# Optimization experiments

Hardware: AMD Instinct MI355X
Metric: run time of the kernel (lower is better)

Reference implementation:

```python
import jax, jax.numpy as jnp
import numpy as np

DIM = 16777216


def spu(z):
    # SPU(x) = x^2 - 0.5 for x >= 0, sigmoid(-x) - 1 for x < 0
    return jnp.where(z >= 0, z * z - 0.5, jax.nn.sigmoid(-z) - 1.0)


def setup_inputs() -> dict:
    key = jax.random.key(0)
    kx, kl, ku = jax.random.split(key, 3)
    x = jax.random.normal(kx, (1, DIM), dtype=jnp.float32)
    l_in = jax.random.normal(kl, (1, DIM), dtype=jnp.float32)
    # guarantee l <= u, with sign crossings so all three branches are exercised
    u_in = l_in + 2.0 * jax.random.uniform(ku, (1, DIM), dtype=jnp.float32)
    return {"x": x, "l_in": l_in, "u_in": u_in}


def reference(x, l_in, u_in):
    x_out = spu(x)
    spu_l = spu(l_in)
    spu_u = spu(u_in)
    # 3-way piecewise box bounds (vectorized _1D_box_bounds):
    #   l >= 0: (spu(l), spu(u)); u <= 0: (spu(u), spu(l)); else: (-0.5, spu(u))
    l_out = jnp.where(l_in >= 0, spu_l, jnp.where(u_in <= 0, spu_u, -0.5))
    u_out = jnp.where(u_in <= 0, spu_l, spu_u)
    return (x_out, l_out, u_out)
```

## Files before the change

### kernel.cpp

```cpp
#include <hip/hip_runtime.h>


typedef float v4f __attribute__((ext_vector_type(4)));

__device__ __forceinline__ float spu_fast(float z) {
    float e   = __expf(z);
    float neg = __builtin_amdgcn_rcpf(1.0f + e) - 1.0f;
    float pos = fmaf(z, z, -0.5f);
    return (z >= 0.0f) ? pos : neg;
}

__global__ __launch_bounds__(256)
void spu_box_kernel(const float* __restrict__ x,
                    const float* __restrict__ l_in,
                    const float* __restrict__ u_in,
                    float* __restrict__ x_out,
                    float* __restrict__ l_out,
                    float* __restrict__ u_out,
                    int n4)
{
    int i = blockIdx.x * blockDim.x + threadIdx.x;
    if (i >= n4) return;

    v4f xv = ((const v4f*)x)[i];
    v4f lv = ((const v4f*)l_in)[i];
    v4f uv = ((const v4f*)u_in)[i];

    v4f xo, lo, uo;

    #pragma unroll
    for (int k = 0; k < 4; ++k) {
        float xs = xv[k];
        float ls = lv[k];
        float us = uv[k];

        float sx = spu_fast(xs);
        float sl = spu_fast(ls);
        float su = spu_fast(us);

        lo[k] = (ls >= 0.0f) ? sl : ((us <= 0.0f) ? su : -0.5f);
        uo[k] = (us <= 0.0f) ? sl : su;
        xo[k] = sx;
    }

    __builtin_nontemporal_store(xo, (v4f*)x_out + i);
    __builtin_nontemporal_store(lo, (v4f*)l_out + i);
    __builtin_nontemporal_store(uo, (v4f*)u_out + i);
}

__global__ void spu_box_tail(const float* __restrict__ x,
                             const float* __restrict__ l_in,
                             const float* __restrict__ u_in,
                             float* __restrict__ x_out,
                             float* __restrict__ l_out,
                             float* __restrict__ u_out,
                             int start, int n)
{
    int i = start + blockIdx.x * blockDim.x + threadIdx.x;
    if (i >= n) return;
    float xs = x[i], ls = l_in[i], us = u_in[i];
    float sx = spu_fast(xs), sl = spu_fast(ls), su = spu_fast(us);
    x_out[i] = sx;
    l_out[i] = (ls >= 0.0f) ? sl : ((us <= 0.0f) ? su : -0.5f);
    u_out[i] = (us <= 0.0f) ? sl : su;
}

extern "C" void kernel_launch(void* const* d_in, const int* in_sizes, int n_in,
                              void* d_out, int out_size, void* d_ws, size_t ws_size,
                              hipStream_t stream) {
    const float* x    = (const float*)d_in[0];
    const float* l_in = (const float*)d_in[1];
    const float* u_in = (const float*)d_in[2];

    const int n = in_sizes[0];
    float* out   = (float*)d_out;
    float* x_out = out;
    float* l_out = out + n;
    float* u_out = out + 2 * (size_t)n;

    const int n4 = n / 4;
    const int block = 256;
    const int grid = (n4 + block - 1) / block;
    spu_box_kernel<<<grid, block, 0, stream>>>(x, l_in, u_in, x_out, l_out, u_out, n4);

    const int tail_start = n4 * 4;
    if (tail_start < n) {
        const int tail = n - tail_start;
        spu_box_tail<<<(tail + 63) / 64, 64, 0, stream>>>(x, l_in, u_in,
                                                          x_out, l_out, u_out,
                                                          tail_start, n);
    }
}
```

Measured before the change: 343.2 us.

## Use grid-stride loop with two-way unroll and drop nontemporal stores

Replaces the one-thread-per-vec4 launch with a grid capped at 2048 blocks that walks the data in a grid-stride loop, processing two vec4 elements per iteration so more loads are in flight per thread. It also swaps the nontemporal stores for ordinary stores. The goal is lower block scheduling overhead and more memory-level parallelism in this bandwidth-bound kernel. The cost is fewer resident waves overall and possible cache pollution from the regular stores.

```diff
diff --git a/kernel.cpp b/kernel.cpp
--- a/kernel.cpp
+++ b/kernel.cpp
@@ -10,42 +10,50 @@
     return (z >= 0.0f) ? pos : neg;
 }
 
-__global__ __launch_bounds__(256)
-void spu_box_kernel(const float* __restrict__ x,
-                    const float* __restrict__ l_in,
-                    const float* __restrict__ u_in,
-                    float* __restrict__ x_out,
-                    float* __restrict__ l_out,
-                    float* __restrict__ u_out,
-                    int n4)
-{
-    int i = blockIdx.x * blockDim.x + threadIdx.x;
-    if (i >= n4) return;
-
-    v4f xv = ((const v4f*)x)[i];
-    v4f lv = ((const v4f*)l_in)[i];
-    v4f uv = ((const v4f*)u_in)[i];
-
-    v4f xo, lo, uo;
-
+__device__ __forceinline__ void spu_box_v4(v4f xv, v4f lv, v4f uv,
+                                           v4f& xo, v4f& lo, v4f& uo) {
     #pragma unroll
     for (int k = 0; k < 4; ++k) {
-        float xs = xv[k];
-        float ls = lv[k];
-        float us = uv[k];
-
+        float xs = xv[k], ls = lv[k], us = uv[k];
         float sx = spu_fast(xs);
         float sl = spu_fast(ls);
         float su = spu_fast(us);
-
         lo[k] = (ls >= 0.0f) ? sl : ((us <= 0.0f) ? su : -0.5f);
         uo[k] = (us <= 0.0f) ? sl : su;
         xo[k] = sx;
     }
+}
 
-    __builtin_nontemporal_store(xo, (v4f*)x_out + i);
-    __builtin_nontemporal_store(lo, (v4f*)l_out + i);
-    __builtin_nontemporal_store(uo, (v4f*)u_out + i);
+__global__ __launch_bounds__(256)
+void spu_box_kernel(const v4f* __restrict__ x4,
+                    const v4f* __restrict__ l4,
+                    const v4f* __restrict__ u4,
+                    v4f* __restrict__ xo4,
+                    v4f* __restrict__ lo4,
+                    v4f* __restrict__ uo4,
+                    int n4)
+{
+    const int stride = gridDim.x * blockDim.x;
+    int i0 = blockIdx.x * blockDim.x + threadIdx.x;
+
+    for (; i0 + stride < n4; i0 += 2 * stride) {
+        const int i1 = i0 + stride;
+        v4f xa = x4[i0], la = l4[i0], ua = u4[i0];
+        v4f xb = x4[i1], lb = l4[i1], ub = u4[i1];
+
+        v4f xoa, loa, uoa, xob, lob, uob;
+        spu_box_v4(xa, la, ua, xoa, loa, uoa);
+        spu_box_v4(xb, lb, ub, xob, lob, uob);
+
+        xo4[i0] = xoa; lo4[i0] = loa; uo4[i0] = uoa;
+        xo4[i1] = xob; lo4[i1] = lob; uo4[i1] = uob;
+    }
+    if (i0 < n4) {
+        v4f xa = x4[i0], la = l4[i0], ua = u4[i0];
+        v4f xoa, loa, uoa;
+        spu_box_v4(xa, la, ua, xoa, loa, uoa);
+        xo4[i0] = xoa; lo4[i0] = loa; uo4[i0] = uoa;
+    }
 }
 
 __global__ void spu_box_tail(const float* __restrict__ x,
@@ -80,8 +88,12 @@
 
     const int n4 = n / 4;
     const int block = 256;
-    const int grid = (n4 + block - 1) / block;
-    spu_box_kernel<<<grid, block, 0, stream>>>(x, l_in, u_in, x_out, l_out, u_out, n4);
+    int grid = (n4 + block - 1) / block;
+    if (grid > 2048) grid = 2048;
+
+    spu_box_kernel<<<grid, block, 0, stream>>>(
+        (const v4f*)x, (const v4f*)l_in, (const v4f*)u_in,
+        (v4f*)x_out, (v4f*)l_out, (v4f*)u_out, n4);
 
     const int tail_start = n4 * 4;
     if (tail_start < n) {
```

After: 334.3 us. 2.6% less time.
